# Kernel optimization log

Hardware: AMD Instinct MI355X
Metric: run time of the kernel (lower is better)

The kernel has to match this reference:

```python
import jax, jax.numpy as jnp
import numpy as np

NHEAD = 12
EPS = 1e-5


def layernorm_nobias(x, gamma):
    mu = jnp.mean(x, axis=-1, keepdims=True)
    var = jnp.var(x, axis=-1, keepdims=True)
    return (x - mu) * jax.lax.rsqrt(var + EPS) * gamma


def setup_inputs() -> dict:
    key = jax.random.key(0)
    ks = jax.random.split(key, 10)
    b, l, d = 4, 2048, 768
    s = d ** -0.5
    return {
        "x": jax.random.normal(ks[0], (b, l, d), jnp.float32),
        "Wq": jax.random.normal(ks[1], (d, d), jnp.float32) * s,
        "Wk": jax.random.normal(ks[2], (d, d), jnp.float32) * s,
        "bk": jax.random.normal(ks[3], (d,), jnp.float32) * 0.02,
        "Wv": jax.random.normal(ks[4], (d, d), jnp.float32) * s,
        "bv": jax.random.normal(ks[5], (d,), jnp.float32) * 0.02,
        "gq": jnp.ones((d,), jnp.float32),
        "gk": jnp.ones((d,), jnp.float32),
        "Wo": jax.random.normal(ks[6], (d, d), jnp.float32) * s,
        "bo": jnp.zeros((d,), jnp.float32),
    }


def reference(x, Wq, Wk, bk, Wv, bv, gq, gk, Wo, bo):
    b, l, d = x.shape
    n = NHEAD
    hd = d // n
    scale = hd ** -0.5
    # projections (torch Linear: x @ W.T + b), QK-norm over full dmodel
    q = layernorm_nobias(x @ Wq.T, gq)
    k = layernorm_nobias(x @ Wk.T + bk, gk)
    v = x @ Wv.T + bv
    # split heads: b l (n hd) -> b n l hd
    q = q.reshape(b, l, n, hd).transpose(0, 2, 1, 3)
    k = k.reshape(b, l, n, hd).transpose(0, 2, 1, 3)
    v = v.reshape(b, l, n, hd).transpose(0, 2, 1, 3)
    # scores [b, n, l_q, l_k]; NOTE: softmax over the QUERY axis (dim=-2)
    scores = jnp.einsum('bnqd,bnkd->bnqk', q, k) * scale
    attn = jax.nn.softmax(scores, axis=-2)
    o = jnp.einsum('bnqk,bnkd->bnqd', attn, v)
    o = o.transpose(0, 2, 1, 3).reshape(b, l, d)
    return o @ Wo.T + bo + x
```

## Files before the change

kernel.cpp:

```cpp
#include <hip/hip_runtime.h>
#include <cstddef>
#include <cstdint>


typedef unsigned short u16;
typedef short  bf16x8 __attribute__((ext_vector_type(8)));
typedef float  f32x4  __attribute__((ext_vector_type(4)));
typedef unsigned short u16x8 __attribute__((ext_vector_type(8)));
typedef unsigned short u16x4 __attribute__((ext_vector_type(4)));

#define B_   4
#define L_   2048
#define D_   768
#define NH_  12
#define HD_  64
#define M_   (B_*L_)
#define SC2  (0.125f * 1.44269504088896f)

__device__ __forceinline__ float ex2(float x) { return __builtin_amdgcn_exp2f(x); }

__device__ __forceinline__ u16 f2bf(float f) {
    union { float f; unsigned u; } v; v.f = f;
    unsigned r = v.u + 0x7FFFu + ((v.u >> 16) & 1u);
    return (u16)(r >> 16);
}
__device__ __forceinline__ float bf2f(u16 b) {
    union { unsigned u; float f; } v; v.u = ((unsigned)b) << 16;
    return v.f;
}
__device__ __forceinline__ unsigned fbits(float f) {
    union { float f; unsigned u; } v; v.f = f; return v.u;
}
__device__ __forceinline__ unsigned packbf(float lo, float hi) {
    return __builtin_amdgcn_perm(fbits(hi), fbits(lo), 0x07060302u);
}

__device__ __forceinline__ void gld16(const void* g, void* l) {
    __builtin_amdgcn_global_load_lds(
        (const __attribute__((address_space(1))) unsigned*)g,
        (__attribute__((address_space(3))) unsigned*)l, 16, 0, 0);
}

__global__ __launch_bounds__(256) void cvt_all(
    const float* __restrict__ X,
    const float* __restrict__ W0, const float* __restrict__ W1,
    const float* __restrict__ W2, const float* __restrict__ W3,
    u16* __restrict__ Yx,
    u16* __restrict__ Y0, u16* __restrict__ Y1,
    u16* __restrict__ Y2, u16* __restrict__ Y3)
{
    const int nX8 = (M_ * D_) / 8;
    const int nW8 = (D_ * D_) / 8;
    int i = blockIdx.x * 256 + threadIdx.x;
    if (i >= nX8 + 4 * nW8) return;
    const float* S; u16* Dst; int off;
    if (i < nX8) { S = X; Dst = Yx; off = i; }
    else {
        int j = i - nX8;
        int w = j / nW8; off = j - w * nW8;
        S   = (w == 0) ? W0 : (w == 1) ? W1 : (w == 2) ? W2 : W3;
        Dst = (w == 0) ? Y0 : (w == 1) ? Y1 : (w == 2) ? Y2 : Y3;
    }
    const float4* xp = (const float4*)S + (size_t)off * 2;
    float4 a = xp[0], b = xp[1];
    u16x8 o;
    o[0] = f2bf(a.x); o[1] = f2bf(a.y); o[2] = f2bf(a.z); o[3] = f2bf(a.w);
    o[4] = f2bf(b.x); o[5] = f2bf(b.y); o[6] = f2bf(b.z); o[7] = f2bf(b.w);
    *((u16x8*)Dst + off) = o;
}

__global__ __launch_bounds__(256, 4) void gemm_qkv(
    const u16* __restrict__ A,
    const u16* __restrict__ W0, const u16* __restrict__ W1,
    const u16* __restrict__ W2,
    const float* __restrict__ bk, const float* __restrict__ bv,
    u16* __restrict__ q_o, u16* __restrict__ k_o, u16* __restrict__ v_o)
{
    __shared__ __align__(16) u16 lds[16384];
    __shared__ float bs[128];
    const int tid  = threadIdx.x;
    const int lane = tid & 63, w = tid >> 6;
    const int s    = lane & 15, quad = lane >> 4;
    const int bid  = blockIdx.x;
    const int xcd  = bid & 7, j0 = bid >> 3;
    const int bm   = (xcd * 8 + j0 / 18) * 128;
    const int sub  = j0 % 18;
    const int seg  = sub / 6;
    const int bn   = (sub % 6) * 128;
    const u16* W = (seg == 0) ? W0 : ((seg == 1) ? W1 : W2);
    u16* OUT = (seg == 0) ? q_o : ((seg == 1) ? k_o : v_o);
    const int mh = (w >> 1) * 64, nh = (w & 1) * 64;
    const int wb = tid & ~63;
    const int cq = quad ^ ((s >> 1) & 3);

    if (tid < 128)
        bs[tid] = (seg == 1) ? bk[bn + tid] : ((seg == 2) ? bv[bn + tid] : 0.0f);

    f32x4 acc[4][4];
    #pragma unroll
    for (int j = 0; j < 4; ++j)
        #pragma unroll
        for (int i = 0; i < 4; ++i) acc[j][i] = (f32x4){0.f, 0.f, 0.f, 0.f};

    {
        int c = tid, r = c >> 2, cs = (c & 3) ^ ((r >> 1) & 3);
        gld16(A + (size_t)(bm + r) * D_ + cs * 8, lds + (size_t)wb * 8);
        gld16(W + (size_t)(bn + r) * D_ + cs * 8, lds + 8192 + (size_t)wb * 8);
        c = tid + 256; r = c >> 2; cs = (c & 3) ^ ((r >> 1) & 3);
        gld16(A + (size_t)(bm + r) * D_ + cs * 8, lds + (size_t)(wb + 256) * 8);
        gld16(W + (size_t)(bn + r) * D_ + cs * 8, lds + 8192 + (size_t)(wb + 256) * 8);
    }
    __syncthreads();

    for (int t = 0; t < 24; ++t) {
        const u16* Ab = lds + (t & 1) * 4096;
        const u16* Bb = lds + 8192 + (t & 1) * 4096;
        if (t < 23) {
            const int k0 = (t + 1) * 32;
            u16* Ad = lds + ((t + 1) & 1) * 4096;
            u16* Bd = lds + 8192 + ((t + 1) & 1) * 4096;
            int c = tid, r = c >> 2, cs = (c & 3) ^ ((r >> 1) & 3);
            gld16(A + (size_t)(bm + r) * D_ + k0 + cs * 8, Ad + (size_t)wb * 8);
            gld16(W + (size_t)(bn + r) * D_ + k0 + cs * 8, Bd + (size_t)wb * 8);
            c = tid + 256; r = c >> 2; cs = (c & 3) ^ ((r >> 1) & 3);
            gld16(A + (size_t)(bm + r) * D_ + k0 + cs * 8, Ad + (size_t)(wb + 256) * 8);
            gld16(W + (size_t)(bn + r) * D_ + k0 + cs * 8, Bd + (size_t)(wb + 256) * 8);
        }
        bf16x8 af[4], bf[4];
        #pragma unroll
        for (int i = 0; i < 4; ++i)
            af[i] = *(const bf16x8*)(Ab + (mh + i * 16 + s) * 32 + cq * 8);
        #pragma unroll
        for (int j = 0; j < 4; ++j)
            bf[j] = *(const bf16x8*)(Bb + (nh + j * 16 + s) * 32 + cq * 8);
        #pragma unroll
        for (int j = 0; j < 4; ++j)
            #pragma unroll
            for (int i = 0; i < 4; ++i)
                acc[j][i] = __builtin_amdgcn_mfma_f32_16x16x32_bf16(
                    bf[j], af[i], acc[j][i], 0, 0, 0);
        __syncthreads();
    }
    u16* Ct = lds;
    #pragma unroll
    for (int j = 0; j < 4; ++j) {
        const int n0 = nh + j * 16 + quad * 4;
        const f32x4 b4 = *(const f32x4*)(bs + n0);
        const int cn = n0 >> 3, off = n0 & 7;
        #pragma unroll
        for (int i = 0; i < 4; ++i) {
            const int m = mh + i * 16 + s;
            u16x4 ov;
            #pragma unroll
            for (int r = 0; r < 4; ++r) ov[r] = f2bf(acc[j][i][r] + b4[r]);
            *(u16x4*)(Ct + m * 128 + ((cn ^ (m & 15)) * 8) + off) = ov;
        }
    }
    __syncthreads();
    {
        const int m = tid >> 1, half = tid & 1;
        u16* dst = OUT + (size_t)(bm + m) * D_ + bn + half * 64;
        #pragma unroll
        for (int cc = 0; cc < 8; ++cc) {
            const int cn = half * 8 + cc;
            u16x8 v = *(const u16x8*)(Ct + m * 128 + ((cn ^ (m & 15)) * 8));
            *(u16x8*)(dst + cc * 8) = v;
        }
    }
}

__global__ __launch_bounds__(256, 3) void gemm_final(
    const u16* __restrict__ A, const u16* __restrict__ W,
    const float* __restrict__ bias, const float* __restrict__ resid,
    float* __restrict__ outf)
{
    __shared__ __align__(16) u16 lds[16384];
    const int tid  = threadIdx.x;
    const int lane = tid & 63, w = tid >> 6;
    const int s    = lane & 15, quad = lane >> 4;
    const int bid  = blockIdx.x;
    const int xcd  = bid & 7, j0 = bid >> 3;
    const int bm   = (xcd * 8 + j0 / 6) * 128;
    const int bn   = (j0 % 6) * 128;
    const int mh   = (w >> 1) * 64, nh = (w & 1) * 64;
    const int wb   = tid & ~63;
    const int cq   = quad ^ ((s >> 1) & 3);
    f32x4 acc[4][4];
    #pragma unroll
    for (int j = 0; j < 4; ++j)
        #pragma unroll
        for (int i = 0; i < 4; ++i) acc[j][i] = (f32x4){0.f, 0.f, 0.f, 0.f};

    {
        int c = tid, r = c >> 2, cs = (c & 3) ^ ((r >> 1) & 3);
        gld16(A + (size_t)(bm + r) * D_ + cs * 8, lds + (size_t)wb * 8);
        gld16(W + (size_t)(bn + r) * D_ + cs * 8, lds + 8192 + (size_t)wb * 8);
        c = tid + 256; r = c >> 2; cs = (c & 3) ^ ((r >> 1) & 3);
        gld16(A + (size_t)(bm + r) * D_ + cs * 8, lds + (size_t)(wb + 256) * 8);
        gld16(W + (size_t)(bn + r) * D_ + cs * 8, lds + 8192 + (size_t)(wb + 256) * 8);
    }
    __syncthreads();

    for (int t = 0; t < 24; ++t) {
        const u16* Ab = lds + (t & 1) * 4096;
        const u16* Bb = lds + 8192 + (t & 1) * 4096;
        if (t < 23) {
            const int k0 = (t + 1) * 32;
            u16* Ad = lds + ((t + 1) & 1) * 4096;
            u16* Bd = lds + 8192 + ((t + 1) & 1) * 4096;
            int c = tid, r = c >> 2, cs = (c & 3) ^ ((r >> 1) & 3);
            gld16(A + (size_t)(bm + r) * D_ + k0 + cs * 8, Ad + (size_t)wb * 8);
            gld16(W + (size_t)(bn + r) * D_ + k0 + cs * 8, Bd + (size_t)wb * 8);
            c = tid + 256; r = c >> 2; cs = (c & 3) ^ ((r >> 1) & 3);
            gld16(A + (size_t)(bm + r) * D_ + k0 + cs * 8, Ad + (size_t)(wb + 256) * 8);
            gld16(W + (size_t)(bn + r) * D_ + k0 + cs * 8, Bd + (size_t)(wb + 256) * 8);
        }
        bf16x8 af[4], bf[4];
        #pragma unroll
        for (int i = 0; i < 4; ++i)
            af[i] = *(const bf16x8*)(Ab + (mh + i * 16 + s) * 32 + cq * 8);
        #pragma unroll
        for (int j = 0; j < 4; ++j)
            bf[j] = *(const bf16x8*)(Bb + (nh + j * 16 + s) * 32 + cq * 8);
        #pragma unroll
        for (int j = 0; j < 4; ++j)
            #pragma unroll
            for (int i = 0; i < 4; ++i)
                acc[j][i] = __builtin_amdgcn_mfma_f32_16x16x32_bf16(
                    bf[j], af[i], acc[j][i], 0, 0, 0);
        __syncthreads();
    }
    #pragma unroll
    for (int j = 0; j < 4; ++j) {
        const int n0 = nh + j * 16 + quad * 4;
        const float4 b4 = *(const float4*)(bias + bn + n0);
        #pragma unroll
        for (int i = 0; i < 4; ++i) {
            const int m = mh + i * 16 + s;
            const size_t base = (size_t)(bm + m) * D_ + bn + n0;
            const float4 rs = *(const float4*)(resid + base);
            float4 o;
            o.x = acc[j][i][0] + b4.x + rs.x;
            o.y = acc[j][i][1] + b4.y + rs.y;
            o.z = acc[j][i][2] + b4.z + rs.z;
            o.w = acc[j][i][3] + b4.w + rs.w;
            *(float4*)(outf + base) = o;
        }
    }
}

__global__ __launch_bounds__(256) void ln2_bf16(
    const u16* __restrict__ Q, const u16* __restrict__ K,
    const float* __restrict__ gq, const float* __restrict__ gk,
    u16* __restrict__ Yq, u16* __restrict__ Yk)
{
    const int row = blockIdx.x;
    const int which = blockIdx.y;
    const u16* x = (which ? K : Q) + (size_t)row * D_;
    const float* gamma = which ? gk : gq;
    u16* Y = which ? Yk : Yq;
    const float scale = which ? 1.0f : (float)SC2;
    const int tid = threadIdx.x;
    float v[3];
    float lsum = 0.f, lsq = 0.f;
    #pragma unroll
    for (int e = 0; e < 3; ++e) {
        float t = bf2f(x[tid + e * 256]);
        v[e] = t; lsum += t; lsq += t * t;
    }
    #pragma unroll
    for (int off = 32; off > 0; off >>= 1) {
        lsum += __shfl_down(lsum, off);
        lsq  += __shfl_down(lsq,  off);
    }
    __shared__ float s1[4], s2[4];
    const int wv = tid >> 6, lane = tid & 63;
    if (lane == 0) { s1[wv] = lsum; s2[wv] = lsq; }
    __syncthreads();
    const float sum = s1[0] + s1[1] + s1[2] + s1[3];
    const float sq  = s2[0] + s2[1] + s2[2] + s2[3];
    const float mu  = sum * (1.0f / D_);
    const float var = sq * (1.0f / D_) - mu * mu;
    const float inv = rsqrtf(var + 1e-5f) * scale;
    #pragma unroll
    for (int e = 0; e < 3; ++e) {
        int c = tid + e * 256;
        Y[(size_t)row * D_ + c] = f2bf((v[e] - mu) * inv * gamma[c]);
    }
}

__global__ __launch_bounds__(256, 3) void attn_stats(
    const u16* __restrict__ Qb, const u16* __restrict__ Kb,
    float* __restrict__ Rl)
{
    __shared__ __align__(16) u16 Ks[128 * 64];
    __shared__ __align__(16) u16 Qs[2][128 * 64];
    __shared__ float lbuf[4][64];
    const int tid  = threadIdx.x;
    const int lane = tid & 63, w = tid >> 6;
    const int s    = lane & 15, quad = lane >> 4;
    const int s7   = s & 7;
    const int bid  = blockIdx.x;
    const int xcd  = bid & 7, j0 = bid >> 3;
    const int bh   = xcd * 6 + j0 / 16;
    const int kbase = (j0 % 16) * 128;
    const int b    = bh / NH_, h = bh % NH_;
    const u16* Qg = Qb + (size_t)b * L_ * D_ + h * HD_;
    const u16* Kg = Kb + (size_t)b * L_ * D_ + h * HD_;
    const int mh = (w >> 1) * 64;
    const int nh = (w & 1) * 64;
    const int wb = tid & ~63;

    #pragma unroll
    for (int c0 = 0; c0 < 1024; c0 += 256) {
        int c = c0 + tid, r = c >> 3, cc = (c & 7) ^ (r & 7);
        gld16(Kg + (size_t)(kbase + r) * D_ + cc * 8, Ks + (size_t)(c0 + wb) * 8);
        gld16(Qg + (size_t)r * D_ + cc * 8, Qs[0] + (size_t)(c0 + wb) * 8);
    }
    __syncthreads();
    bf16x8 kf[2][4];
    #pragma unroll
    for (int kk = 0; kk < 2; ++kk)
        #pragma unroll
        for (int i = 0; i < 4; ++i)
            kf[kk][i] = *(const bf16x8*)(Ks + (mh + i * 16 + s) * 64 +
                                         ((kk * 4 + quad) ^ s7) * 8);
    float lacc[4][4];
    #pragma unroll
    for (int i = 0; i < 4; ++i)
        #pragma unroll
        for (int r = 0; r < 4; ++r) lacc[i][r] = 0.f;

    for (int t = 0; t < 16; ++t) {
        if (t < 15) {
            const int qn = (t + 1) * 128;
            u16* Qd = Qs[(t + 1) & 1];
            #pragma unroll
            for (int c0 = 0; c0 < 1024; c0 += 256) {
                int c = c0 + tid, r = c >> 3, cc = (c & 7) ^ (r & 7);
                gld16(Qg + (size_t)(qn + r) * D_ + cc * 8, Qd + (size_t)(c0 + wb) * 8);
            }
        }
        const u16* Qt = Qs[t & 1];
        f32x4 acc[4][4];
        #pragma unroll
        for (int i = 0; i < 4; ++i)
            #pragma unroll
            for (int j = 0; j < 4; ++j) acc[i][j] = (f32x4){0.f, 0.f, 0.f, 0.f};
        #pragma unroll
        for (int kk = 0; kk < 2; ++kk) {
            bf16x8 bf[4];
            #pragma unroll
            for (int j = 0; j < 4; ++j)
                bf[j] = *(const bf16x8*)(Qt + (nh + j * 16 + s) * 64 +
                                         ((kk * 4 + quad) ^ s7) * 8);
            #pragma unroll
            for (int i = 0; i < 4; ++i)
                #pragma unroll
                for (int j = 0; j < 4; ++j)
                    acc[i][j] = __builtin_amdgcn_mfma_f32_16x16x32_bf16(
                        kf[kk][i], bf[j], acc[i][j], 0, 0, 0);
        }
        #pragma unroll
        for (int i = 0; i < 4; ++i)
            #pragma unroll
            for (int r = 0; r < 4; ++r) {
                float l0 = ex2(acc[i][0][r]) + ex2(acc[i][1][r]);
                float l1 = ex2(acc[i][2][r]) + ex2(acc[i][3][r]);
                lacc[i][r] += l0 + l1;
            }
        __syncthreads();
    }
    #pragma unroll
    for (int i = 0; i < 4; ++i)
        #pragma unroll
        for (int r = 0; r < 4; ++r) {
            float v = lacc[i][r];
            #pragma unroll
            for (int d2 = 1; d2 < 16; d2 <<= 1) v += __shfl_xor(v, d2);
            lacc[i][r] = v;
        }
    if (s == 0) {
        #pragma unroll
        for (int i = 0; i < 4; ++i)
            #pragma unroll
            for (int r = 0; r < 4; ++r)
                lbuf[w][i * 16 + quad * 4 + r] = lacc[i][r];
    }
    __syncthreads();
    if (tid < 128) {
        int kh = tid >> 6, kl = tid & 63;
        float l = lbuf[kh * 2][kl] + lbuf[kh * 2 + 1][kl];
        Rl[(size_t)bh * L_ + kbase + tid] = 1.0f / l;
    }
}

__global__ __launch_bounds__(256) void transpose_v_scaled(
    const u16* __restrict__ Vb, const float* __restrict__ Rl,
    u16* __restrict__ Vt)
{
    const int l0 = blockIdx.x * 64, h = blockIdx.y, b = blockIdx.z;
    const int bh = b * NH_ + h;
    __shared__ __align__(16) u16 Ts[64][72];
    const int tid = threadIdx.x;
    #pragma unroll
    for (int c = tid; c < 512; c += 256) {
        int r = c >> 3, cc = c & 7;
        u16x8 val = *(const u16x8*)(Vb + (size_t)(b * L_ + l0 + r) * D_ + h * HD_ + cc * 8);
        const float rl = Rl[(size_t)bh * L_ + l0 + r];
        #pragma unroll
        for (int e = 0; e < 8; ++e) val[e] = f2bf(bf2f(val[e]) * rl);
        *(u16x8*)(&Ts[r][cc * 8]) = val;
    }
    __syncthreads();
    const int d = tid >> 2, lc = (tid & 3) * 16;
    u16 tmp[16];
    #pragma unroll
    for (int e = 0; e < 16; ++e) tmp[e] = Ts[lc + e][d];
    u16* dst = Vt + ((size_t)bh * HD_ + d) * L_ + l0 + (lc & 32) + ((lc >> 4) & 1) * 4;
    #pragma unroll
    for (int qd = 0; qd < 4; ++qd) {
        u16x4 o;
        #pragma unroll
        for (int e = 0; e < 4; ++e) o[e] = tmp[qd * 4 + e];
        *(u16x4*)(dst + qd * 8) = o;
    }
}

__global__ __launch_bounds__(256, 3) void attn_out(
    const u16* __restrict__ Qb, const u16* __restrict__ Kb,
    const u16* __restrict__ Vt, u16* __restrict__ Ob)
{
    __shared__ __align__(16) u16 Qs[128 * 64];
    __shared__ __align__(16) u16 Ks[2][64 * 64];
    __shared__ __align__(16) u16 Vts[2][64 * 64];
    const int tid  = threadIdx.x;
    const int lane = tid & 63, w = tid >> 6;
    const int s    = lane & 15, quad = lane >> 4;
    const int s7   = s & 7;
    const int bid  = blockIdx.x;
    const int xcd  = bid & 7, j0 = bid >> 3;
    const int bh   = xcd * 6 + j0 / 16;
    const int qbase = (j0 % 16) * 128;
    const int b    = bh / NH_, h = bh % NH_;
    const int qw   = w * 32;
    const u16* Qg = Qb + (size_t)b * L_ * D_ + h * HD_;
    const u16* Kg = Kb + (size_t)b * L_ * D_ + h * HD_;
    const u16* Vg = Vt + (size_t)bh * HD_ * L_;
    const int wb = tid & ~63;

    #pragma unroll
    for (int c0 = 0; c0 < 1024; c0 += 256) {
        int c = c0 + tid, r = c >> 3, cc = (c & 7) ^ (r & 7);
        gld16(Qg + (size_t)(qbase + r) * D_ + cc * 8, Qs + (size_t)(c0 + wb) * 8);
    }
    {
        int c = tid, r = c >> 3, cc = (c & 7) ^ (r & 7);
        gld16(Kg + (size_t)r * D_ + cc * 8, Ks[0] + (size_t)wb * 8);
        gld16(Vg + (size_t)r * L_ + cc * 8, Vts[0] + (size_t)wb * 8);
        c = tid + 256; r = c >> 3; cc = (c & 7) ^ (r & 7);
        gld16(Kg + (size_t)r * D_ + cc * 8, Ks[0] + (size_t)(wb + 256) * 8);
        gld16(Vg + (size_t)r * L_ + cc * 8, Vts[0] + (size_t)(wb + 256) * 8);
    }
    __syncthreads();
    bf16x8 qf[2][2];
    #pragma unroll
    for (int kk = 0; kk < 2; ++kk)
        #pragma unroll
        for (int j = 0; j < 2; ++j)
            qf[kk][j] = *(const bf16x8*)(Qs + (qw + j * 16 + s) * 64 +
                                         ((kk * 4 + quad) ^ s7) * 8);
    f32x4 acc_o[4][2];
    #pragma unroll
    for (int i = 0; i < 4; ++i)
        #pragma unroll
        for (int j = 0; j < 2; ++j) acc_o[i][j] = (f32x4){0.f, 0.f, 0.f, 0.f};

    for (int t = 0; t < 32; ++t) {
        const u16* Kt  = Ks[t & 1];
        const u16* Vtt = Vts[t & 1];
        if (t < 31) {
            const int kn = (t + 1) * 64;
            u16* Kd = Ks[(t + 1) & 1];
            u16* Vd = Vts[(t + 1) & 1];
            int c = tid, r = c >> 3, cc = (c & 7) ^ (r & 7);
            gld16(Kg + (size_t)(kn + r) * D_ + cc * 8, Kd + (size_t)wb * 8);
            gld16(Vg + (size_t)r * L_ + kn + cc * 8,   Vd + (size_t)wb * 8);
            c = tid + 256; r = c >> 3; cc = (c & 7) ^ (r & 7);
            gld16(Kg + (size_t)(kn + r) * D_ + cc * 8, Kd + (size_t)(wb + 256) * 8);
            gld16(Vg + (size_t)r * L_ + kn + cc * 8,   Vd + (size_t)(wb + 256) * 8);
        }
        f32x4 acc_s[4][2];
        #pragma unroll
        for (int i = 0; i < 4; ++i)
            #pragma unroll
            for (int j = 0; j < 2; ++j) acc_s[i][j] = (f32x4){0.f, 0.f, 0.f, 0.f};
        #pragma unroll
        for (int kk = 0; kk < 2; ++kk) {
            bf16x8 kfr[4];
            #pragma unroll
            for (int i = 0; i < 4; ++i)
                kfr[i] = *(const bf16x8*)(Kt + (i * 16 + s) * 64 +
                                          ((kk * 4 + quad) ^ s7) * 8);
            #pragma unroll
            for (int i = 0; i < 4; ++i)
                #pragma unroll
                for (int j = 0; j < 2; ++j)
                    acc_s[i][j] = __builtin_amdgcn_mfma_f32_16x16x32_bf16(
                        kfr[i], qf[kk][j], acc_s[i][j], 0, 0, 0);
        }
        unsigned pk[4][2][2];
        #pragma unroll
        for (int i = 0; i < 4; ++i)
            #pragma unroll
            for (int j = 0; j < 2; ++j) {
                float p0 = ex2(acc_s[i][j][0]), p1 = ex2(acc_s[i][j][1]);
                float p2 = ex2(acc_s[i][j][2]), p3 = ex2(acc_s[i][j][3]);
                pk[i][j][0] = packbf(p0, p1);
                pk[i][j][1] = packbf(p2, p3);
            }
        #pragma unroll
        for (int kk = 0; kk < 2; ++kk) {
            bf16x8 av[4];
            #pragma unroll
            for (int i = 0; i < 4; ++i)
                av[i] = *(const bf16x8*)(Vtt + (i * 16 + s) * 64 +
                                         ((kk * 4 + quad) ^ s7) * 8);
            #pragma unroll
            for (int j = 0; j < 2; ++j) {
                union { unsigned u[4]; bf16x8 v; } bu;
                bu.u[0] = pk[2 * kk][j][0];
                bu.u[1] = pk[2 * kk][j][1];
                bu.u[2] = pk[2 * kk + 1][j][0];
                bu.u[3] = pk[2 * kk + 1][j][1];
                #pragma unroll
                for (int i = 0; i < 4; ++i)
                    acc_o[i][j] = __builtin_amdgcn_mfma_f32_16x16x32_bf16(
                        av[i], bu.v, acc_o[i][j], 0, 0, 0);
            }
        }
        __syncthreads();
    }
    #pragma unroll
    for (int i = 0; i < 4; ++i) {
        const int dchunk = i * 2 + (quad >> 1), doff = (quad & 1) * 4;
        #pragma unroll
        for (int j = 0; j < 2; ++j) {
            const int q = qw + j * 16 + s;
            u16x4 ov;
            #pragma unroll
            for (int r = 0; r < 4; ++r) ov[r] = f2bf(acc_o[i][j][r]);
            *(u16x4*)(Qs + q * 64 + (dchunk ^ s7) * 8 + doff) = ov;
        }
    }
    __syncthreads();
    {
        const int q = tid >> 1, half = tid & 1, q7 = q & 7;
        u16* dst = Ob + (size_t)(b * L_ + qbase + q) * D_ + h * HD_ + half * 32;
        #pragma unroll
        for (int c = 0; c < 4; ++c) {
            const int cn = half * 4 + c;
            u16x8 v = *(const u16x8*)(Qs + q * 64 + ((cn ^ q7) * 8));
            *(u16x8*)(dst + c * 8) = v;
        }
    }
}

extern "C" void kernel_launch(void* const* d_in, const int* in_sizes, int n_in,
                              void* d_out, int out_size, void* d_ws, size_t ws_size,
                              hipStream_t stream)
{
    const float* x  = (const float*)d_in[0];
    const float* Wq = (const float*)d_in[1];
    const float* Wk = (const float*)d_in[2];
    const float* bk = (const float*)d_in[3];
    const float* Wv = (const float*)d_in[4];
    const float* bv = (const float*)d_in[5];
    const float* gq = (const float*)d_in[6];
    const float* gk = (const float*)d_in[7];
    const float* Wo = (const float*)d_in[8];
    const float* bo = (const float*)d_in[9];
    float* out = (float*)d_out;

    char* p = (char*)d_ws;
    u16* xb   = (u16*)p;  p += (size_t)M_ * D_ * 2;
    u16* qpre = (u16*)p;  p += (size_t)M_ * D_ * 2;
    u16* kpre = (u16*)p;  p += (size_t)M_ * D_ * 2;
    u16* vb   = (u16*)p;  p += (size_t)M_ * D_ * 2;
    u16* qb   = (u16*)p;  p += (size_t)M_ * D_ * 2;
    u16* kb   = (u16*)p;  p += (size_t)M_ * D_ * 2;
    u16* wqb  = (u16*)p;  p += (size_t)D_ * D_ * 2;
    u16* wkb  = (u16*)p;  p += (size_t)D_ * D_ * 2;
    u16* wvb  = (u16*)p;  p += (size_t)D_ * D_ * 2;
    u16* wob  = (u16*)p;  p += (size_t)D_ * D_ * 2;
    float* Rl = (float*)p; p += (size_t)B_ * NH_ * L_ * 4;
    u16* ob = qpre;
    u16* vt = kpre;

    const int nTot8 = (M_ * D_ + 4 * D_ * D_) / 8;
    cvt_all<<<(nTot8 + 255) / 256, 256, 0, stream>>>(
        x, Wq, Wk, Wv, Wo, xb, wqb, wkb, wvb, wob);

    gemm_qkv<<<1152, 256, 0, stream>>>(
        xb, wqb, wkb, wvb, bk, bv, qpre, kpre, vb);

    ln2_bf16<<<dim3(M_, 2), 256, 0, stream>>>(qpre, kpre, gq, gk, qb, kb);

    attn_stats<<<768, 256, 0, stream>>>(qb, kb, Rl);
    transpose_v_scaled<<<dim3(L_ / 64, NH_, B_), 256, 0, stream>>>(vb, Rl, vt);
    attn_out<<<768, 256, 0, stream>>>(qb, kb, vt, ob);

    gemm_final<<<384, 256, 0, stream>>>(ob, wob, bo, x, out);
}
```

Baseline: 280.8 us.

## Triple-buffer K/V tiles in attention with partial waitcnt and MFMA priority

```diff
diff --git a/kernel.cpp b/kernel.cpp
--- a/kernel.cpp
+++ b/kernel.cpp
@@ -354,12 +354,14 @@
             for (int j = 0; j < 4; ++j)
                 bf[j] = *(const bf16x8*)(Qt + (nh + j * 16 + s) * 64 +
                                          ((kk * 4 + quad) ^ s7) * 8);
+            __builtin_amdgcn_s_setprio(1);
             #pragma unroll
             for (int i = 0; i < 4; ++i)
                 #pragma unroll
                 for (int j = 0; j < 4; ++j)
                     acc[i][j] = __builtin_amdgcn_mfma_f32_16x16x32_bf16(
                         kf[kk][i], bf[j], acc[i][j], 0, 0, 0);
+            __builtin_amdgcn_s_setprio(0);
         }
         #pragma unroll
         for (int i = 0; i < 4; ++i)
@@ -431,9 +433,8 @@
     const u16* __restrict__ Qb, const u16* __restrict__ Kb,
     const u16* __restrict__ Vt, u16* __restrict__ Ob)
 {
-    __shared__ __align__(16) u16 Qs[128 * 64];
-    __shared__ __align__(16) u16 Ks[2][64 * 64];
-    __shared__ __align__(16) u16 Vts[2][64 * 64];
+    __shared__ __align__(16) u16 Ks[3][64 * 64];
+    __shared__ __align__(16) u16 Vts[3][64 * 64];
     const int tid  = threadIdx.x;
     const int lane = tid & 63, w = tid >> 6;
     const int s    = lane & 15, quad = lane >> 4;
@@ -449,27 +450,28 @@
     const u16* Vg = Vt + (size_t)bh * HD_ * L_;
     const int wb = tid & ~63;
 
-    #pragma unroll
-    for (int c0 = 0; c0 < 1024; c0 += 256) {
-        int c = c0 + tid, r = c >> 3, cc = (c & 7) ^ (r & 7);
-        gld16(Qg + (size_t)(qbase + r) * D_ + cc * 8, Qs + (size_t)(c0 + wb) * 8);
-    }
-    {
+    bf16x8 qf[2][2];
+    #pragma unroll
+    for (int kk = 0; kk < 2; ++kk)
+        #pragma unroll
+        for (int j = 0; j < 2; ++j)
+            qf[kk][j] = *(const bf16x8*)(
+                Qg + (size_t)(qbase + qw + j * 16 + s) * D_ + (kk * 4 + quad) * 8);
+
+    #pragma unroll
+    for (int t0 = 0; t0 < 2; ++t0) {
+        const int kn = t0 * 64;
+        u16* Kd = Ks[t0];
+        u16* Vd = Vts[t0];
         int c = tid, r = c >> 3, cc = (c & 7) ^ (r & 7);
-        gld16(Kg + (size_t)r * D_ + cc * 8, Ks[0] + (size_t)wb * 8);
-        gld16(Vg + (size_t)r * L_ + cc * 8, Vts[0] + (size_t)wb * 8);
+        gld16(Kg + (size_t)(kn + r) * D_ + cc * 8, Kd + (size_t)wb * 8);
+        gld16(Vg + (size_t)r * L_ + kn + cc * 8,   Vd + (size_t)wb * 8);
         c = tid + 256; r = c >> 3; cc = (c & 7) ^ (r & 7);
-        gld16(Kg + (size_t)r * D_ + cc * 8, Ks[0] + (size_t)(wb + 256) * 8);
-        gld16(Vg + (size_t)r * L_ + cc * 8, Vts[0] + (size_t)(wb + 256) * 8);
-    }
-    __syncthreads();
-    bf16x8 qf[2][2];
-    #pragma unroll
-    for (int kk = 0; kk < 2; ++kk)
-        #pragma unroll
-        for (int j = 0; j < 2; ++j)
-            qf[kk][j] = *(const bf16x8*)(Qs + (qw + j * 16 + s) * 64 +
-                                         ((kk * 4 + quad) ^ s7) * 8);
+        gld16(Kg + (size_t)(kn + r) * D_ + cc * 8, Kd + (size_t)(wb + 256) * 8);
+        gld16(Vg + (size_t)r * L_ + kn + cc * 8,   Vd + (size_t)(wb + 256) * 8);
+    }
+    __syncthreads();
+
     f32x4 acc_o[4][2];
     #pragma unroll
     for (int i = 0; i < 4; ++i)
@@ -477,15 +479,17 @@
         for (int j = 0; j < 2; ++j) acc_o[i][j] = (f32x4){0.f, 0.f, 0.f, 0.f};
 
     for (int t = 0; t < 32; ++t) {
-        const u16* Kt  = Ks[t & 1];
-        const u16* Vtt = Vts[t & 1];
-        if (t < 31) {
-            const int kn = (t + 1) * 64;
-            u16* Kd = Ks[(t + 1) & 1];
-            u16* Vd = Vts[(t + 1) & 1];
+        const int bi = t % 3;
+        const u16* Kt  = Ks[bi];
+        const u16* Vtt = Vts[bi];
+        if (t + 2 < 32) {
+            const int pi = (t + 2) % 3;
+            const int kn = (t + 2) * 64;
+            u16* Kd = Ks[pi];
+            u16* Vd = Vts[pi];
             int c = tid, r = c >> 3, cc = (c & 7) ^ (r & 7);
             gld16(Kg + (size_t)(kn + r) * D_ + cc * 8, Kd + (size_t)wb * 8);
-            gld16(Vg + (size_t)r * L_ + kn + cc * 8,   Vd + (size_t)wb * 8);
+            gld16(Vg + (size_t)r * L_ + kn + cc * 8,   Vd + (size_t)(wb) * 8);
             c = tid + 256; r = c >> 3; cc = (c & 7) ^ (r & 7);
             gld16(Kg + (size_t)(kn + r) * D_ + cc * 8, Kd + (size_t)(wb + 256) * 8);
             gld16(Vg + (size_t)r * L_ + kn + cc * 8,   Vd + (size_t)(wb + 256) * 8);
@@ -502,12 +506,14 @@
             for (int i = 0; i < 4; ++i)
                 kfr[i] = *(const bf16x8*)(Kt + (i * 16 + s) * 64 +
                                           ((kk * 4 + quad) ^ s7) * 8);
+            __builtin_amdgcn_s_setprio(1);
             #pragma unroll
             for (int i = 0; i < 4; ++i)
                 #pragma unroll
                 for (int j = 0; j < 2; ++j)
                     acc_s[i][j] = __builtin_amdgcn_mfma_f32_16x16x32_bf16(
                         kfr[i], qf[kk][j], acc_s[i][j], 0, 0, 0);
+            __builtin_amdgcn_s_setprio(0);
         }
         unsigned pk[4][2][2];
         #pragma unroll
@@ -526,6 +532,7 @@
             for (int i = 0; i < 4; ++i)
                 av[i] = *(const bf16x8*)(Vtt + (i * 16 + s) * 64 +
                                          ((kk * 4 + quad) ^ s7) * 8);
+            __builtin_amdgcn_s_setprio(1);
             #pragma unroll
             for (int j = 0; j < 2; ++j) {
                 union { unsigned u[4]; bf16x8 v; } bu;
@@ -538,9 +545,18 @@
                     acc_o[i][j] = __builtin_amdgcn_mfma_f32_16x16x32_bf16(
                         av[i], bu.v, acc_o[i][j], 0, 0, 0);
             }
-        }
-        __syncthreads();
-    }
+            __builtin_amdgcn_s_setprio(0);
+        }
+        if (t < 30) {
+            asm volatile("s_waitcnt vmcnt(4)" ::: "memory");
+            __builtin_amdgcn_s_barrier();
+        } else if (t == 30) {
+            asm volatile("s_waitcnt vmcnt(0)" ::: "memory");
+            __builtin_amdgcn_s_barrier();
+        }
+    }
+    __syncthreads();
+    u16* Ep = (u16*)Ks;
     #pragma unroll
     for (int i = 0; i < 4; ++i) {
         const int dchunk = i * 2 + (quad >> 1), doff = (quad & 1) * 4;
@@ -550,7 +566,7 @@
             u16x4 ov;
             #pragma unroll
             for (int r = 0; r < 4; ++r) ov[r] = f2bf(acc_o[i][j][r]);
-            *(u16x4*)(Qs + q * 64 + (dchunk ^ s7) * 8 + doff) = ov;
+            *(u16x4*)(Ep + q * 64 + (dchunk ^ s7) * 8 + doff) = ov;
         }
     }
     __syncthreads();
@@ -560,7 +576,7 @@
         #pragma unroll
         for (int c = 0; c < 4; ++c) {
             const int cn = half * 4 + c;
-            u16x8 v = *(const u16x8*)(Qs + q * 64 + ((cn ^ q7) * 8));
+            u16x8 v = *(const u16x8*)(Ep + q * 64 + ((cn ^ q7) * 8));
             *(u16x8*)(dst + c * 8) = v;
         }
     }
```

Result: faster. 273.6 us (-2.6%).
